# Optimization experiments

Measured on AMD Instinct MI355X. Metric: run time of the kernel, lower is better.

## Reference

```python
import jax, jax.numpy as jnp
import numpy as np
from jax import lax

B, T, H, M, K, Q, P = 32, 128, 256, 1000, 3, 4, 2  # batch, phones, hidden, max_mel_len, kernel, q_out, p_out


def _ln(x, g, b, eps=1e-5):
    mu = jnp.mean(x, -1, keepdims=True)
    var = jnp.mean((x - mu) ** 2, -1, keepdims=True)
    return (x - mu) * lax.rsqrt(var + eps) * g + b


def _forward(x, x_mask, x_dur, params):
    (proj_w, proj_b, conv_w, conv_b, conv_g, conv_beta,
     q_w1, q_b1, q_g, q_beta, q_w2, q_b2,
     p_w1, p_b1, p_g, p_beta, p_w2, p_b2,
     proj1_w, proj1_b, proj2_w, proj2_b, projo_w, projo_b) = params

    valid = (~x_mask).astype(x.dtype)[:, :, None]                      # (B,T,1), 1 = real phone
    # proj -> ConvBlock (shared between the w and c branches; dropout is identity in eval)
    h = x @ proj_w + proj_b                                            # (B,T,H)
    hc = lax.conv_general_dilated((h * valid).transpose(0, 2, 1), conv_w,
                                  (1,), 'SAME',
                                  dimension_numbers=('NCH', 'OIH', 'NCH'))
    hc = hc.transpose(0, 2, 1) + conv_b                                # (B,T,8)
    hc = jax.nn.silu(_ln(hc, conv_g, conv_beta)) * valid               # (B,T,8)

    mel_lens = jnp.minimum(jnp.round(jnp.sum(x_dur, -1)).astype(jnp.int32), M)
    mel_pad = jnp.arange(M)[None, :] >= mel_lens[:, None]              # (B,M) True = padded frame
    mask = x_mask[:, None, :] | mel_pad[:, :, None]                    # (B,M,T)

    e = jnp.cumsum(x_dur, -1)                                          # phone end times
    s = e - x_dur                                                      # phone start times
    t = jnp.arange(1, M + 1, dtype=x.dtype)
    E = jnp.where(mask, 0.0, e[:, None, :] - t[None, :, None])         # (B,M,T)
    S = jnp.where(mask, 0.0, t[None, :, None] - s[:, None, :])         # (B,M,T)

    feat = jnp.concatenate([jnp.broadcast_to(hc[:, None], (B, M, T, 8)),
                            S[..., None], E[..., None]], axis=-1)      # (B,M,T,10)

    # mlp_q scores -> masked softmax over phone axis
    sc = jax.nn.silu(_ln(feat @ q_w1 + q_b1, q_g, q_beta)) @ q_w2 + q_b2   # (B,M,T,Q)
    sc = jnp.where(x_mask[:, None, :, None], -jnp.inf, sc)
    w = jax.nn.softmax(sc, axis=2)
    w = jnp.where(mel_pad[:, :, None, None], 0.0, w)                   # (B,M,T,Q)

    # mlp_p per-(frame,phone) auxiliary features
    c = jax.nn.silu(_ln(feat @ p_w1 + p_b1, p_g, p_beta)) @ p_w2 + p_b2    # (B,M,T,P)

    # dual einsum combine (matches torch permute+view ordering: q-major then feature)
    wh = jnp.einsum('bmnq,bnh->bmqh', w, x).reshape(B, M, Q * H) @ proj1_w + proj1_b
    wc = jnp.einsum('bmnq,bmnp->bmqp', w, c).reshape(B, M, Q * P) @ proj2_w + proj2_b
    o = jnp.where(mel_pad[:, :, None], 0.0, wh + wc) @ projo_w + projo_b   # (B,M,2H)

    mel_mask = jnp.broadcast_to(mel_pad[:, :, None], (B, M, T))
    return o, mel_mask, mel_lens, jnp.transpose(w, (0, 3, 1, 2))


def setup_inputs() -> dict:
    key = jax.random.key(0)
    ks = jax.random.split(key, 16)
    x = jax.random.normal(ks[0], (B, T, H), jnp.float32)
    x_lengths = jax.random.randint(ks[1], (B,), T // 2, T + 1).at[0].set(T)
    x_mask = jnp.arange(T)[None, :] >= x_lengths[:, None]              # True = pad
    x_dur = jax.random.uniform(ks[2], (B, T), jnp.float32, 2.0, 10.0)
    x_dur = x_dur * (~x_mask)
    x_dur = x_dur.at[0].multiply(2.0)  # element 0 total duration > M -> static max_mel_len = M

    def xavier(k, shape):
        return jax.random.normal(k, shape, jnp.float32) * jnp.sqrt(2.0 / (shape[0] + shape[1]))

    return dict(
        x=x, x_mask=x_mask, x_dur=x_dur, x_lengths=x_lengths,
        proj_w=xavier(ks[3], (H, H)), proj_b=jnp.zeros((H,)),
        conv_w=jax.random.normal(ks[4], (8, H, K), jnp.float32) * 0.05, conv_b=jnp.zeros((8,)),
        conv_g=jnp.ones((8,)), conv_beta=jnp.zeros((8,)),
        q_w1=xavier(ks[5], (10, Q)), q_b1=jnp.zeros((Q,)),
        q_g=jnp.ones((Q,)), q_beta=jnp.zeros((Q,)),
        q_w2=xavier(ks[6], (Q, Q)), q_b2=jnp.zeros((Q,)),
        p_w1=xavier(ks[7], (10, P)), p_b1=jnp.zeros((P,)),
        p_g=jnp.ones((P,)), p_beta=jnp.zeros((P,)),
        p_w2=xavier(ks[8], (P, P)), p_b2=jnp.zeros((P,)),
        proj1_w=xavier(ks[9], (H * Q, H)), proj1_b=jnp.zeros((H,)),
        proj2_w=xavier(ks[10], (Q * P, H)), proj2_b=jnp.zeros((H,)),
        projo_w=xavier(ks[11], (H, 2 * H)), projo_b=jnp.zeros((2 * H,)),
    )


def reference(x, x_mask, x_dur, x_lengths,
              proj_w, proj_b, conv_w, conv_b, conv_g, conv_beta,
              q_w1, q_b1, q_g, q_beta, q_w2, q_b2,
              p_w1, p_b1, p_g, p_beta, p_w2, p_b2,
              proj1_w, proj1_b, proj2_w, proj2_b, projo_w, projo_b):
    params = (proj_w, proj_b, conv_w, conv_b, conv_g, conv_beta,
              q_w1, q_b1, q_g, q_beta, q_w2, q_b2,
              p_w1, p_b1, p_g, p_beta, p_w2, p_b2,
              proj1_w, proj1_b, proj2_w, proj2_b, projo_w, projo_b)
    return _forward(x, x_mask, x_dur, params)
```

## Files before the change

kernel.cpp:

```cpp
#include <hip/hip_runtime.h>
#include <math.h>

#define BB 32
#define TT 128
#define HH 256
#define MM 1000

typedef __attribute__((ext_vector_type(8))) short short8;
typedef __attribute__((ext_vector_type(4))) float floatx4;

__device__ inline void fma4(float4& a, const float4 b, float s) {
    a.x += b.x * s; a.y += b.y * s; a.z += b.z * s; a.w += b.w * s;
}

__device__ inline unsigned short f2bf(float f) {
    union { float f; unsigned int u; } c; c.f = f;
    unsigned int u = c.u;
    return (unsigned short)((u + 0x7FFFu + ((u >> 16) & 1u)) >> 16);
}

__device__ inline float bf2f(unsigned short h) {
    union { unsigned int u; float f; } c; c.u = ((unsigned int)h) << 16; return c.f;
}


__global__ void k_prep(const float* __restrict__ dur, float* __restrict__ e_cum,
                       int* __restrict__ ml_i, float* __restrict__ ml_out,
                       unsigned short* __restrict__ w_bf) {
    int b = blockIdx.x;
    int tid = threadIdx.x;
    #pragma unroll
    for (int q = 0; q < 4; ++q) {
        uint4* dst = (uint4*)(w_bf + (((size_t)(b * 4 + q)) * 1024 + 1000) * 128);
        for (int e = tid; e < 384; e += 64) dst[e] = make_uint4(0, 0, 0, 0);
    }
    if (tid == 0) {
        float run = 0.f;
        const float* d = dur + b * TT;
        float* e = e_cum + b * TT;
        for (int t = 0; t < TT; ++t) { run += d[t]; e[t] = run; }
        int ml = (int)rintf(run);
        if (ml > MM) ml = MM;
        if (ml < 0) ml = 0;
        ml_i[b] = ml;
        ml_out[b] = (float)ml;
    }
}

__global__ __launch_bounds__(256) void k_h(const float* __restrict__ x,
                                           const float* __restrict__ pw,
                                           const float* __restrict__ pb,
                                           float* __restrict__ h) {
    __shared__ float xs[16][HH];
    int blk = blockIdx.x;
    int b = blk >> 3, tt = blk & 7;
    int t0 = tt * 16;
    int tid = threadIdx.x;
    for (int e = tid; e < 16 * HH; e += 256) {
        int r = e >> 8, i = e & 255;
        xs[r][i] = x[(b * TT + t0 + r) * HH + i];
    }
    __syncthreads();
    int jg = tid & 63, rg = tid >> 6;
    int j4 = jg * 4;
    float4 bias = *(const float4*)(pb + j4);
    float4 acc[4];
    #pragma unroll
    for (int ri = 0; ri < 4; ++ri) acc[ri] = bias;
    #pragma unroll 4
    for (int i = 0; i < HH; ++i) {
        float4 wv = *(const float4*)(pw + i * HH + j4);
        #pragma unroll
        for (int ri = 0; ri < 4; ++ri) fma4(acc[ri], wv, xs[rg * 4 + ri][i]);
    }
    #pragma unroll
    for (int ri = 0; ri < 4; ++ri)
        *(float4*)(h + (b * TT + t0 + rg * 4 + ri) * HH + j4) = acc[ri];
}

__global__ __launch_bounds__(128) void k_conv(const float* __restrict__ h,
                                              const float* __restrict__ cw,
                                              const int* __restrict__ xlen,
                                              float* __restrict__ hcpre) {
    __shared__ float hs[18][257];
    __shared__ float cws[8][769];
    int blk = blockIdx.x;
    int b = blk >> 3, tt = blk & 7;
    int t0 = tt * 16;
    int tid = threadIdx.x;
    int L = xlen[b];
    for (int e = tid; e < 18 * 256; e += 128) {
        int r = e >> 8, i = e & 255;
        int t = t0 - 1 + r;
        float v = 0.f;
        if (t >= 0 && t < TT && t < L) v = h[((size_t)b * TT + t) * HH + i];
        hs[r][i] = v;
    }
    for (int e = tid; e < 6144; e += 128) {
        int o = e / 768, rem = e - o * 768;
        cws[o][rem] = cw[e];
    }
    __syncthreads();
    int o = tid >> 4, tl = tid & 15;
    float acc = 0.f;
    #pragma unroll
    for (int k = 0; k < 3; ++k) {
        const float* wr = &cws[o][k];
        const float* hr = hs[tl + k];
        #pragma unroll 8
        for (int i = 0; i < 256; ++i) acc += hr[i] * wr[i * 3];
    }
    hcpre[((size_t)b * TT + t0 + tl) * 8 + o] = acc;
}

__global__ __launch_bounds__(128) void k_bases(
    const float* __restrict__ hcpre, const float* __restrict__ cb,
    const float* __restrict__ cg, const float* __restrict__ cbeta,
    const float* __restrict__ qw1, const float* __restrict__ qb1,
    const float* __restrict__ pw1, const float* __restrict__ pb1,
    const float* __restrict__ e_cum, const float* __restrict__ dur,
    const int* __restrict__ xlen,
    float* __restrict__ baseq, float* __restrict__ basep) {
    int b = blockIdx.x;
    int t = threadIdx.x;
    int L = xlen[b];
    float v[8];
    float mu = 0.f;
    #pragma unroll
    for (int o = 0; o < 8; ++o) { v[o] = hcpre[(b * TT + t) * 8 + o] + cb[o]; mu += v[o]; }
    mu *= 0.125f;
    float var = 0.f;
    #pragma unroll
    for (int o = 0; o < 8; ++o) { float d = v[o] - mu; var += d * d; }
    var *= 0.125f;
    float rs = 1.0f / sqrtf(var + 1e-5f);
    float valid = (t < L) ? 1.f : 0.f;
    #pragma unroll
    for (int o = 0; o < 8; ++o) {
        float a = (v[o] - mu) * rs * cg[o] + cbeta[o];
        v[o] = a / (1.f + expf(-a)) * valid;
    }
    float e = e_cum[b * TT + t];
    float s_ = e - dur[b * TT + t];
    #pragma unroll
    for (int j = 0; j < 4; ++j) {
        float acc = qb1[j];
        #pragma unroll
        for (int o = 0; o < 8; ++o) acc += v[o] * qw1[o * 4 + j];
        acc += e * qw1[9 * 4 + j] - s_ * qw1[8 * 4 + j];
        baseq[(b * TT + t) * 4 + j] = acc;
    }
    #pragma unroll
    for (int j = 0; j < 2; ++j) {
        float acc = pb1[j];
        #pragma unroll
        for (int o = 0; o < 8; ++o) acc += v[o] * pw1[o * 2 + j];
        acc += e * pw1[9 * 2 + j] - s_ * pw1[8 * 2 + j];
        basep[(b * TT + t) * 2 + j] = acc;
    }
}

__global__ __launch_bounds__(256) void k_wsoft(
    const float* __restrict__ baseq, const float* __restrict__ basep,
    const float* __restrict__ qw1, const float* __restrict__ qg,
    const float* __restrict__ qbeta, const float* __restrict__ qw2,
    const float* __restrict__ qb2,
    const float* __restrict__ pw1, const float* __restrict__ pg,
    const float* __restrict__ pbeta, const float* __restrict__ pw2,
    const float* __restrict__ pb2,
    const int* __restrict__ xlen, const int* __restrict__ ml_i,
    float* __restrict__ w_out, float* __restrict__ mm_out,
    float* __restrict__ wc8, unsigned short* __restrict__ w_bf) {
    int blk = blockIdx.x;
    int b = blk / 250;
    int mg = blk - b * 250;
    int wv = threadIdx.x >> 6, lane = threadIdx.x & 63;
    int m = mg * 4 + wv;
    int ml = ml_i[b];
    int t1 = lane, t2 = lane + 64;
    bool pad = (m >= ml);
    size_t mmbase = ((size_t)b * MM + m) * TT;
    mm_out[mmbase + t1] = pad ? 1.f : 0.f;
    mm_out[mmbase + t2] = pad ? 1.f : 0.f;
    if (pad) {
        #pragma unroll
        for (int q = 0; q < 4; ++q) {
            size_t wb = ((size_t)(b * 4 + q) * MM + m) * TT;
            w_out[wb + t1] = 0.f;
            w_out[wb + t2] = 0.f;
            unsigned short* wbq = w_bf + (((size_t)(b * 4 + q)) * 1024 + m) * 128;
            wbq[t1] = 0; wbq[t2] = 0;
        }
        if (lane == 0) {
            #pragma unroll
            for (int r = 0; r < 8; ++r) wc8[((size_t)b * MM + m) * 8 + r] = 0.f;
        }
        return;
    }
    int L = xlen[b];
    float mp1 = (float)(m + 1);
    float dq[4];
    #pragma unroll
    for (int j = 0; j < 4; ++j) dq[j] = mp1 * (qw1[8 * 4 + j] - qw1[9 * 4 + j]);

    float sc1[4], sc2[4];
    float c1v[2], c2v[2];
    #pragma unroll
    for (int half = 0; half < 2; ++half) {
        int t = half ? t2 : t1;
        float* sc = half ? sc2 : sc1;
        float* cv = half ? c2v : c1v;
        if (t < L) {
            float4 bq = *(const float4*)(baseq + ((size_t)b * TT + t) * 4);
            float z[4] = {bq.x + dq[0], bq.y + dq[1], bq.z + dq[2], bq.w + dq[3]};
            float mu = 0.25f * (z[0] + z[1] + z[2] + z[3]);
            float var = 0.f;
            #pragma unroll
            for (int j = 0; j < 4; ++j) { float d = z[j] - mu; var += d * d; }
            var *= 0.25f;
            float rs = 1.f / sqrtf(var + 1e-5f);
            float a[4];
            #pragma unroll
            for (int j = 0; j < 4; ++j) {
                float av = (z[j] - mu) * rs * qg[j] + qbeta[j];
                a[j] = av / (1.f + expf(-av));
            }
            #pragma unroll
            for (int q = 0; q < 4; ++q) {
                float s = qb2[q];
                #pragma unroll
                for (int j = 0; j < 4; ++j) s += a[j] * qw2[j * 4 + q];
                sc[q] = s;
            }
            float z0 = basep[((size_t)b * TT + t) * 2 + 0] + mp1 * (pw1[16] - pw1[18]);
            float z1 = basep[((size_t)b * TT + t) * 2 + 1] + mp1 * (pw1[17] - pw1[19]);
            float pmu = 0.5f * (z0 + z1);
            float d0 = z0 - pmu, d1 = z1 - pmu;
            float pvar = 0.5f * (d0 * d0 + d1 * d1);
            float prs = 1.f / sqrtf(pvar + 1e-5f);
            float a0 = d0 * prs * pg[0] + pbeta[0];
            float a1 = d1 * prs * pg[1] + pbeta[1];
            a0 = a0 / (1.f + expf(-a0));
            a1 = a1 / (1.f + expf(-a1));
            cv[0] = pb2[0] + a0 * pw2[0] + a1 * pw2[2];
            cv[1] = pb2[1] + a0 * pw2[1] + a1 * pw2[3];
        } else {
            sc[0] = sc[1] = sc[2] = sc[3] = -__builtin_inff();
            cv[0] = cv[1] = 0.f;
        }
    }
    float w1[4], w2[4];
    #pragma unroll
    for (int q = 0; q < 4; ++q) {
        float mx = fmaxf(sc1[q], sc2[q]);
        #pragma unroll
        for (int off = 32; off > 0; off >>= 1) mx = fmaxf(mx, __shfl_xor(mx, off, 64));
        float e1 = expf(sc1[q] - mx);
        float e2 = expf(sc2[q] - mx);
        float s = e1 + e2;
        #pragma unroll
        for (int off = 32; off > 0; off >>= 1) s += __shfl_xor(s, off, 64);
        w1[q] = e1 / s;
        w2[q] = e2 / s;
        size_t wb = ((size_t)(b * 4 + q) * MM + m) * TT;
        w_out[wb + t1] = w1[q];
        w_out[wb + t2] = w2[q];
        unsigned short* wbq = w_bf + (((size_t)(b * 4 + q)) * 1024 + m) * 128;
        wbq[t1] = f2bf(w1[q]);
        wbq[t2] = f2bf(w2[q]);
    }
    float red[8];
    #pragma unroll
    for (int r8 = 0; r8 < 8; ++r8) {
        int q = r8 >> 1, p = r8 & 1;
        float v = w1[q] * c1v[p] + w2[q] * c2v[p];
        #pragma unroll
        for (int off = 32; off > 0; off >>= 1) v += __shfl_xor(v, off, 64);
        red[r8] = v;
    }
    if (lane == 0) {
        #pragma unroll
        for (int r8 = 0; r8 < 8; ++r8) wc8[((size_t)b * MM + m) * 8 + r8] = red[r8];
    }
}

__global__ __launch_bounds__(256) void k_pw_part(const float* __restrict__ p1w,
                                                 const float* __restrict__ po,
                                                 float* __restrict__ PWpart) {
    __shared__ float S[16][64];
    int blk = blockIdx.x;
    int ks = blk & 3, colT = (blk >> 2) & 7, ht = blk >> 5;
    int q = colT >> 1, j0 = (colT & 1) * 256;
    int h0 = ht * 16, k0 = ks * 64;
    int tid = threadIdx.x;
    for (int e = tid; e < 1024; e += 256) {
        int r = e >> 6, c = e & 63;
        S[r][c] = p1w[(q * 256 + h0 + r) * 256 + k0 + c];
    }
    __syncthreads();
    int jg = tid & 63, rg = tid >> 6;
    int jcol = j0 + jg * 4;
    float4 acc[4];
    #pragma unroll
    for (int r = 0; r < 4; ++r) acc[r] = make_float4(0, 0, 0, 0);
    float4 nb = *(const float4*)(po + (size_t)k0 * 512 + jcol);
    for (int c = 0; c < 64; ++c) {
        float4 cur = nb;
        if (c < 63) nb = *(const float4*)(po + (size_t)(k0 + c + 1) * 512 + jcol);
        #pragma unroll
        for (int r = 0; r < 4; ++r) fma4(acc[r], cur, S[rg * 4 + r][c]);
    }
    #pragma unroll
    for (int r = 0; r < 4; ++r) {
        int hh = h0 + rg * 4 + r;
        *(float4*)(PWpart + (size_t)ks * 524288 + hh * 2048 + q * 512 + jcol) = acc[r];
    }
}

__global__ __launch_bounds__(256) void k_pwt(const float* __restrict__ PWpart,
                                             unsigned short* __restrict__ pwh,
                                             unsigned short* __restrict__ pwl) {
    __shared__ float S[64][65];
    int blk = blockIdx.x;
    int nt = blk & 31, ct = blk >> 5;
    int c0 = ct * 64, n0 = nt * 64;
    int tid = threadIdx.x;
    for (int e = tid; e < 4096; e += 256) {
        int cc = e >> 6, nn = e & 63;
        size_t off = (size_t)(c0 + cc) * 2048 + n0 + nn;
        float v = PWpart[off] + PWpart[524288 + off]
                + PWpart[2 * 524288 + off] + PWpart[3 * 524288 + off];
        S[cc][nn] = v;
    }
    __syncthreads();
    for (int e = tid; e < 4096; e += 256) {
        int nn = e >> 6, cc = e & 63;
        float v = S[cc][nn];
        unsigned short h = f2bf(v);
        size_t d = (size_t)(n0 + nn) * 256 + c0 + cc;
        pwh[d] = h;
        pwl[d] = f2bf(v - bf2f(h));
    }
}

__global__ __launch_bounds__(256) void k_xcvt(const float* __restrict__ x,
                                              unsigned short* __restrict__ xh,
                                              unsigned short* __restrict__ xl) {
    int idx = (blockIdx.x * 256 + threadIdx.x) * 4;
    float4 v = *(const float4*)(x + idx);
    float vv[4] = {v.x, v.y, v.z, v.w};
    union { unsigned short us[4]; uint2 u; } hi, lo;
    #pragma unroll
    for (int k = 0; k < 4; ++k) {
        unsigned short h = f2bf(vv[k]);
        hi.us[k] = h;
        lo.us[k] = f2bf(vv[k] - bf2f(h));
    }
    *(uint2*)(xh + idx) = hi.u;
    *(uint2*)(xl + idx) = lo.u;
}

__global__ __launch_bounds__(512) void k_small(const float* __restrict__ p2w,
    const float* __restrict__ po, const float* __restrict__ p1b,
    const float* __restrict__ p2b, const float* __restrict__ pob,
    float* __restrict__ P2o, float* __restrict__ bvec) {
    int j = threadIdx.x;
    float acc[9];
    #pragma unroll
    for (int r = 0; r < 9; ++r) acc[r] = 0.f;
    for (int c = 0; c < HH; ++c) {
        float pv = po[c * 512 + j];
        #pragma unroll
        for (int r = 0; r < 8; ++r) acc[r] += p2w[r * HH + c] * pv;
        acc[8] += (p1b[c] + p2b[c]) * pv;
    }
    #pragma unroll
    for (int r = 0; r < 8; ++r) P2o[r * 512 + j] = acc[r];
    bvec[j] = acc[8] + pob[j];
}

__device__ inline int swzk(int row, int chunk) {
    return row * 32 + ((chunk ^ ((row >> 1) & 3)) << 3);
}

__global__ __launch_bounds__(256) void k_A2m(const unsigned short* __restrict__ xh,
                                             const unsigned short* __restrict__ xl,
                                             const unsigned short* __restrict__ pwh,
                                             const unsigned short* __restrict__ pwl,
                                             unsigned short* __restrict__ A2T) {
    __shared__ __align__(16) unsigned short SM[16384];
    unsigned short* Ah = SM;
    unsigned short* Al = SM + 4096;
    unsigned short* Bh = SM + 8192;
    unsigned short* Bl = SM + 12288;
    int blk = blockIdx.x;
    int b = blk >> 4, nt = blk & 15;
    int n0 = nt * 128;
    int tid = threadIdx.x;
    int lane = tid & 63, wv = tid >> 6;
    int wm = wv & 1, wn = wv >> 1;

    floatx4 acc[16];
    #pragma unroll
    for (int i = 0; i < 16; ++i) acc[i] = (floatx4){0.f, 0.f, 0.f, 0.f};

    int srow = tid >> 1, shalf = tid & 1;
    const unsigned short* gxh = xh + ((size_t)(b * TT + srow) * 256 + shalf * 16);
    const unsigned short* gxl = xl + ((size_t)(b * TT + srow) * 256 + shalf * 16);
    const unsigned short* gph = pwh + ((size_t)(n0 + srow) * 256 + shalf * 16);
    const unsigned short* gpl = pwl + ((size_t)(n0 + srow) * 256 + shalf * 16);
    int wAd0 = swzk(srow, 2 * shalf);
    int wAd1 = swzk(srow, 2 * shalf + 1);

    int ra = wm * 64 + (lane & 15);
    int rb = wn * 64 + (lane & 15);
    int cq = lane >> 4;

    for (int kc = 0; kc < 256; kc += 32) {
        uint4 a0 = *(const uint4*)(gxh + kc);
        uint4 a1 = *(const uint4*)(gxh + kc + 8);
        uint4 a2 = *(const uint4*)(gxl + kc);
        uint4 a3 = *(const uint4*)(gxl + kc + 8);
        uint4 b0 = *(const uint4*)(gph + kc);
        uint4 b1 = *(const uint4*)(gph + kc + 8);
        uint4 b2 = *(const uint4*)(gpl + kc);
        uint4 b3 = *(const uint4*)(gpl + kc + 8);
        *(uint4*)&Ah[wAd0] = a0; *(uint4*)&Ah[wAd1] = a1;
        *(uint4*)&Al[wAd0] = a2; *(uint4*)&Al[wAd1] = a3;
        *(uint4*)&Bh[wAd0] = b0; *(uint4*)&Bh[wAd1] = b1;
        *(uint4*)&Bl[wAd0] = b2; *(uint4*)&Bl[wAd1] = b3;
        __syncthreads();
        short8 afh[4], afl[4], bfh[4], bfl[4];
        #pragma unroll
        for (int i = 0; i < 4; ++i) {
            afh[i] = *(const short8*)&Ah[swzk(ra + i * 16, cq)];
            afl[i] = *(const short8*)&Al[swzk(ra + i * 16, cq)];
            bfh[i] = *(const short8*)&Bh[swzk(rb + i * 16, cq)];
            bfl[i] = *(const short8*)&Bl[swzk(rb + i * 16, cq)];
        }
        #pragma unroll
        for (int i = 0; i < 4; ++i)
            #pragma unroll
            for (int j = 0; j < 4; ++j) {
                floatx4 c = acc[i * 4 + j];
                c = __builtin_amdgcn_mfma_f32_16x16x32_bf16(afh[i], bfh[j], c, 0, 0, 0);
                c = __builtin_amdgcn_mfma_f32_16x16x32_bf16(afh[i], bfl[j], c, 0, 0, 0);
                c = __builtin_amdgcn_mfma_f32_16x16x32_bf16(afl[i], bfh[j], c, 0, 0, 0);
                acc[i * 4 + j] = c;
            }
        __syncthreads();
    }

    unsigned short* OT = SM;
    #pragma unroll
    for (int i = 0; i < 4; ++i)
        #pragma unroll
        for (int j = 0; j < 4; ++j) {
            int nloc = wn * 64 + j * 16 + (lane & 15);
            int tb = wm * 64 + i * 16 + ((lane >> 4) << 2);
            union { unsigned short us[4]; uint2 v; } pk;
            #pragma unroll
            for (int r = 0; r < 4; ++r) pk.us[r] = f2bf(acc[i * 4 + j][r]);
            int chunk = tb >> 3, sub = tb & 7;
            *(uint2*)&OT[nloc * 128 + (((chunk ^ (nloc & 15)) << 3) | sub)] = pk.v;
        }
    __syncthreads();
    int q = n0 >> 9, jb = n0 & 511;
    for (int u = tid; u < 2048; u += 256) {
        int nrow = u >> 4, seg = u & 15;
        uint4 v = *(const uint4*)&OT[nrow * 128 + ((seg ^ (nrow & 15)) << 3)];
        *(uint4*)(A2T + (((size_t)(b * 4 + q) * 512) + jb + nrow) * 128 + seg * 8) = v;
    }
}

__global__ __launch_bounds__(256, 2) void k_main(
    const unsigned short* __restrict__ w_bf, const unsigned short* __restrict__ A2T,
    const float* __restrict__ wc8, const float* __restrict__ P2o,
    const float* __restrict__ bvec, const float* __restrict__ pob,
    const int* __restrict__ ml_i, float* __restrict__ o_out) {
    __shared__ __align__(16) unsigned short Asm[128 * 128];
    __shared__ __align__(16) unsigned short Bsm[128 * 128];
    int blk = blockIdx.x;
    int nt = blk & 3, mt = (blk >> 2) & 7, b = blk >> 5;
    int m0 = mt * 128, n0 = nt * 128;
    int tid = threadIdx.x;
    int lane = tid & 63, wv = tid >> 6;
    int wm = wv & 1, wn = wv >> 1;

    floatx4 acc[16];
    #pragma unroll
    for (int i = 0; i < 16; ++i) acc[i] = (floatx4){0.f, 0.f, 0.f, 0.f};

    int rl = lane >> 4;
    int cl = lane & 15;
    int ra = wm * 64 + cl;
    int rb = wn * 64 + cl;

    for (int q = 0; q < 4; ++q) {
        uint4 la[8], lb[8];
        #pragma unroll
        for (int j = 0; j < 8; ++j) {
            int e = tid + j * 256;
            int row = e >> 4, chunk = e & 15;
            la[j] = *(const uint4*)(w_bf +
                (((size_t)(b * 4 + q)) * 1024 + m0 + row) * 128 + chunk * 8);
            lb[j] = *(const uint4*)(A2T +
                (((size_t)(b * 4 + q)) * 512 + n0 + row) * 128 + chunk * 8);
        }
        if (q) __syncthreads();
        #pragma unroll
        for (int j = 0; j < 8; ++j) {
            int e = tid + j * 256;
            int row = e >> 4, chunk = e & 15;
            int d = row * 128 + ((chunk ^ (row & 15)) << 3);
            *(uint4*)&Asm[d] = la[j];
            *(uint4*)&Bsm[d] = lb[j];
        }
        __syncthreads();
        #pragma unroll
        for (int kk = 0; kk < 4; ++kk) {
            int csw = ((kk * 4 + rl) ^ cl) << 3;
            short8 af[4], bfr[4];
            #pragma unroll
            for (int i = 0; i < 4; ++i)
                af[i] = *(const short8*)&Asm[(ra + i * 16) * 128 + csw];
            #pragma unroll
            for (int j2 = 0; j2 < 4; ++j2)
                bfr[j2] = *(const short8*)&Bsm[(rb + j2 * 16) * 128 + csw];
            #pragma unroll
            for (int i = 0; i < 4; ++i)
                #pragma unroll
                for (int j2 = 0; j2 < 4; ++j2)
                    acc[i * 4 + j2] = __builtin_amdgcn_mfma_f32_16x16x32_bf16(
                        af[i], bfr[j2], acc[i * 4 + j2], 0, 0, 0);
        }
    }
    __syncthreads();

    float* wc8s = (float*)Asm;
    float* P2os = (float*)Bsm;
    float* bvs  = (float*)Bsm + 1024;
    float* pobs = (float*)Bsm + 1152;
    for (int e = tid; e < 1024; e += 256) {
        int mm_ = e >> 3, r = e & 7;
        int m = m0 + mm_;
        wc8s[e] = (m < MM) ? wc8[((size_t)b * MM + m) * 8 + r] : 0.f;
    }
    for (int e = tid; e < 1024; e += 256) {
        int r = e >> 7, j = e & 127;
        P2os[e] = P2o[r * 512 + n0 + j];
    }
    if (tid < 128) {
        bvs[tid] = bvec[n0 + tid];
        pobs[tid] = pob[n0 + tid];
    }
    __syncthreads();
    int ml = ml_i[b];
    #pragma unroll
    for (int i = 0; i < 4; ++i) {
        #pragma unroll
        for (int j = 0; j < 4; ++j) {
            int nloc = wn * 64 + j * 16 + (lane & 15);
            #pragma unroll
            for (int reg = 0; reg < 4; ++reg) {
                int mloc = wm * 64 + i * 16 + (lane >> 4) * 4 + reg;
                int m = m0 + mloc;
                if (m >= MM) continue;
                float v;
                if (m < ml) {
                    v = acc[i * 4 + j][reg] + bvs[nloc];
                    #pragma unroll
                    for (int r8 = 0; r8 < 8; ++r8)
                        v += wc8s[mloc * 8 + r8] * P2os[r8 * 128 + nloc];
                } else {
                    v = pobs[nloc];
                }
                o_out[((size_t)b * MM + m) * 512 + n0 + nloc] = v;
            }
        }
    }
}

extern "C" void kernel_launch(void* const* d_in, const int* in_sizes, int n_in,
                              void* d_out, int out_size, void* d_ws, size_t ws_size,
                              hipStream_t stream) {
    (void)in_sizes; (void)n_in; (void)out_size; (void)ws_size;
    const float* x      = (const float*)d_in[0];
    const float* dur    = (const float*)d_in[2];
    const int*   xlen   = (const int*)d_in[3];
    const float* proj_w = (const float*)d_in[4];
    const float* proj_b = (const float*)d_in[5];
    const float* conv_w = (const float*)d_in[6];
    const float* conv_b = (const float*)d_in[7];
    const float* conv_g = (const float*)d_in[8];
    const float* conv_be= (const float*)d_in[9];
    const float* q_w1   = (const float*)d_in[10];
    const float* q_b1   = (const float*)d_in[11];
    const float* q_g    = (const float*)d_in[12];
    const float* q_be   = (const float*)d_in[13];
    const float* q_w2   = (const float*)d_in[14];
    const float* q_b2   = (const float*)d_in[15];
    const float* p_w1   = (const float*)d_in[16];
    const float* p_b1   = (const float*)d_in[17];
    const float* p_g    = (const float*)d_in[18];
    const float* p_be   = (const float*)d_in[19];
    const float* p_w2   = (const float*)d_in[20];
    const float* p_b2   = (const float*)d_in[21];
    const float* p1w    = (const float*)d_in[22];
    const float* p1b    = (const float*)d_in[23];
    const float* p2w    = (const float*)d_in[24];
    const float* p2b    = (const float*)d_in[25];
    const float* pow_   = (const float*)d_in[26];
    const float* pob    = (const float*)d_in[27];

    float* ws    = (float*)d_ws;
    float* e_cum = ws + 0;
    float* hcpre = ws + 4096;
    float* baseq = ws + 36864;
    float* basep = ws + 53248;
    float* h     = ws + 61440;
    unsigned short* x_hi = (unsigned short*)(ws + 61440);
    unsigned short* x_lo = (unsigned short*)(ws + 585728);
    unsigned short* pw_h = (unsigned short*)(ws + 1110016);
    unsigned short* pw_l = (unsigned short*)(ws + 1372160);
    unsigned short* A2T = (unsigned short*)(ws + 1634304);
    float* wc8   = ws + 5828608;
    float* P2o   = ws + 6084608;
    float* bvec  = ws + 6088704;
    int*   ml_i  = (int*)(ws + 6089216);
    float* PWpart= ws + 6090752;
    unsigned short* w_bf = (unsigned short*)(ws + 8187904);

    float* o_out  = (float*)d_out;
    float* mm_out = o_out + 16384000;
    float* ml_out = o_out + 20480000;
    float* w_out  = o_out + 20480032;

    k_prep<<<dim3(BB), dim3(64), 0, stream>>>(dur, e_cum, ml_i, ml_out, w_bf);
    k_h<<<dim3(BB * 8), dim3(256), 0, stream>>>(x, proj_w, proj_b, h);
    k_conv<<<dim3(BB * 8), dim3(128), 0, stream>>>(h, conv_w, xlen, hcpre);
    k_xcvt<<<dim3(1024), dim3(256), 0, stream>>>(x, x_hi, x_lo);
    k_bases<<<dim3(BB), dim3(128), 0, stream>>>(hcpre, conv_b, conv_g, conv_be,
                                                q_w1, q_b1, p_w1, p_b1,
                                                e_cum, dur, xlen, baseq, basep);
    k_pw_part<<<dim3(512), dim3(256), 0, stream>>>(p1w, pow_, PWpart);
    k_pwt<<<dim3(128), dim3(256), 0, stream>>>(PWpart, pw_h, pw_l);
    k_small<<<dim3(1), dim3(512), 0, stream>>>(p2w, pow_, p1b, p2b, pob, P2o, bvec);
    k_A2m<<<dim3(512), dim3(256), 0, stream>>>(x_hi, x_lo, pw_h, pw_l, A2T);
    k_wsoft<<<dim3(BB * 250), dim3(256), 0, stream>>>(baseq, basep,
                                                      q_w1, q_g, q_be, q_w2, q_b2,
                                                      p_w1, p_g, p_be, p_w2, p_b2,
                                                      xlen, ml_i, w_out, mm_out, wc8, w_bf);
    k_main<<<dim3(BB * 32), dim3(256), 0, stream>>>(w_bf, A2T, wc8, P2o, bvec,
                                                    pob, ml_i, o_out);
}
```

Baseline: 454.1 us.

## Double-buffer k_main GEMM tiles in half-K stages with padded LDS rows

Splits each 128-wide K tile of the main GEMM into two 64-wide stages and double-buffers them in LDS. The next stage's global loads are issued before the current stage's MFMAs run, overlapping memory latency with compute. The XOR swizzle is replaced with 72-element padded rows to avoid bank conflicts. Each stage is smaller, so there are twice as many barriers. LDS footprint is slightly larger (2x2x128x72 shorts), which may affect the 2-blocks-per-CU occupancy target.

Measured after the change: 402.5 us. -11.4%, faster.

```diff
diff --git a/kernel.cpp b/kernel.cpp
--- a/kernel.cpp
+++ b/kernel.cpp
@@ -478,8 +478,8 @@
     const float* __restrict__ wc8, const float* __restrict__ P2o,
     const float* __restrict__ bvec, const float* __restrict__ pob,
     const int* __restrict__ ml_i, float* __restrict__ o_out) {
-    __shared__ __align__(16) unsigned short Asm[128 * 128];
-    __shared__ __align__(16) unsigned short Bsm[128 * 128];
+    __shared__ __align__(16) unsigned short Asm[2][128 * 72];
+    __shared__ __align__(16) unsigned short Bsm[2][128 * 72];
     int blk = blockIdx.x;
     int nt = blk & 3, mt = (blk >> 2) & 7, b = blk >> 5;
     int m0 = mt * 128, n0 = nt * 128;
@@ -496,37 +496,44 @@
     int ra = wm * 64 + cl;
     int rb = wn * 64 + cl;
 
-    for (int q = 0; q < 4; ++q) {
-        uint4 la[8], lb[8];
-        #pragma unroll
-        for (int j = 0; j < 8; ++j) {
-            int e = tid + j * 256;
-            int row = e >> 4, chunk = e & 15;
-            la[j] = *(const uint4*)(w_bf +
-                (((size_t)(b * 4 + q)) * 1024 + m0 + row) * 128 + chunk * 8);
-            lb[j] = *(const uint4*)(A2T +
-                (((size_t)(b * 4 + q)) * 512 + n0 + row) * 128 + chunk * 8);
-        }
-        if (q) __syncthreads();
-        #pragma unroll
-        for (int j = 0; j < 8; ++j) {
-            int e = tid + j * 256;
-            int row = e >> 4, chunk = e & 15;
-            int d = row * 128 + ((chunk ^ (row & 15)) << 3);
-            *(uint4*)&Asm[d] = la[j];
-            *(uint4*)&Bsm[d] = lb[j];
-        }
-        __syncthreads();
-        #pragma unroll
-        for (int kk = 0; kk < 4; ++kk) {
-            int csw = ((kk * 4 + rl) ^ cl) << 3;
+    int srow = tid >> 3, schunk = tid & 7;
+    int doff = srow * 72 + schunk * 8;
+    const size_t bq4 = (size_t)b * 4;
+
+    #pragma unroll
+    for (int j = 0; j < 4; ++j) {
+        int row = srow + j * 32;
+        uint4 va = *(const uint4*)(w_bf + ((bq4 + 0) * 1024 + m0 + row) * 128 + schunk * 8);
+        uint4 vb = *(const uint4*)(A2T + ((bq4 + 0) * 512 + n0 + row) * 128 + schunk * 8);
+        *(uint4*)&Asm[0][doff + j * 2304] = va;
+        *(uint4*)&Bsm[0][doff + j * 2304] = vb;
+    }
+    __syncthreads();
+
+    int cur = 0;
+    for (int s = 0; s < 8; ++s) {
+        uint4 la[4], lb[4];
+        if (s < 7) {
+            int q = (s + 1) >> 1, half = (s + 1) & 1;
+            #pragma unroll
+            for (int j = 0; j < 4; ++j) {
+                int row = srow + j * 32;
+                la[j] = *(const uint4*)(w_bf +
+                    ((bq4 + q) * 1024 + m0 + row) * 128 + half * 64 + schunk * 8);
+                lb[j] = *(const uint4*)(A2T +
+                    ((bq4 + q) * 512 + n0 + row) * 128 + half * 64 + schunk * 8);
+            }
+        }
+        #pragma unroll
+        for (int kk = 0; kk < 2; ++kk) {
+            int co = (kk * 4 + rl) * 8;
             short8 af[4], bfr[4];
             #pragma unroll
             for (int i = 0; i < 4; ++i)
-                af[i] = *(const short8*)&Asm[(ra + i * 16) * 128 + csw];
+                af[i] = *(const short8*)&Asm[cur][(ra + i * 16) * 72 + co];
             #pragma unroll
             for (int j2 = 0; j2 < 4; ++j2)
-                bfr[j2] = *(const short8*)&Bsm[(rb + j2 * 16) * 128 + csw];
+                bfr[j2] = *(const short8*)&Bsm[cur][(rb + j2 * 16) * 72 + co];
             #pragma unroll
             for (int i = 0; i < 4; ++i)
                 #pragma unroll
@@ -534,13 +541,21 @@
                     acc[i * 4 + j2] = __builtin_amdgcn_mfma_f32_16x16x32_bf16(
                         af[i], bfr[j2], acc[i * 4 + j2], 0, 0, 0);
         }
-    }
-    __syncthreads();
-
-    float* wc8s = (float*)Asm;
-    float* P2os = (float*)Bsm;
-    float* bvs  = (float*)Bsm + 1024;
-    float* pobs = (float*)Bsm + 1152;
+        if (s < 7) {
+            #pragma unroll
+            for (int j = 0; j < 4; ++j) {
+                *(uint4*)&Asm[cur ^ 1][doff + j * 2304] = la[j];
+                *(uint4*)&Bsm[cur ^ 1][doff + j * 2304] = lb[j];
+            }
+        }
+        __syncthreads();
+        cur ^= 1;
+    }
+
+    float* wc8s = (float*)&Asm[0][0];
+    float* P2os = (float*)&Bsm[0][0];
+    float* bvs  = (float*)&Bsm[0][0] + 1024;
+    float* pobs = (float*)&Bsm[0][0] + 1152;
     for (int e = tid; e < 1024; e += 256) {
         int mm_ = e >> 3, r = e & 7;
         int m = m0 + mm_;
```
